# Performance work log

Hardware: AMD Instinct MI355X
Metric: run time of the kernel (lower is better)

## Reference

```python
import jax, jax.numpy as jnp
import numpy as np

LN_EPS = 1e-12
BIG = 1e30
BAND = 15  # end index may be at most 15 tokens after start


def output_layer(x, w1, b1, g, b, w2, b2):
    # Linear -> ReLU -> LayerNorm -> Linear (dropout is identity at eval)
    h = jax.nn.relu(x @ w1 + b1)
    mu = jnp.mean(h, axis=-1, keepdims=True)
    var = jnp.mean(jnp.square(h - mu), axis=-1, keepdims=True)
    h = (h - mu) * jax.lax.rsqrt(var + LN_EPS) * g + b
    return h @ w2 + b2


def setup_inputs() -> dict:
    key = jax.random.key(0)
    ks = jax.random.split(key, 8)
    B, S, D = 8, 4096, 1024
    H2 = 2 * D
    inp = {
        "context_input": jax.random.normal(ks[0], (B, S, D), jnp.float32),
        "context_mask": jnp.ones((B, S), jnp.float32),
    }
    def head(k1, k2, n_ans):
        return (
            0.02 * jax.random.normal(k1, (D, H2), jnp.float32),
            jnp.zeros((H2,), jnp.float32),
            jnp.ones((H2,), jnp.float32),
            jnp.zeros((H2,), jnp.float32),
            0.02 * jax.random.normal(k2, (H2, n_ans), jnp.float32),
            jnp.zeros((n_ans,), jnp.float32),
        )
    for name, k1, k2, n_ans in [("start", ks[1], ks[2], 1), ("end", ks[3], ks[4], 1), ("type", ks[5], ks[6], 4)]:
        w1, b1, g, b, w2, b2 = head(k1, k2, n_ans)
        inp[f"{name}_w1"] = w1; inp[f"{name}_b1"] = b1
        inp[f"{name}_g"] = g; inp[f"{name}_b"] = b
        inp[f"{name}_w2"] = w2; inp[f"{name}_b2"] = b2
    return inp


def reference(context_input, context_mask,
              start_w1, start_b1, start_g, start_b, start_w2, start_b2,
              end_w1, end_b1, end_g, end_b, end_w2, end_b2,
              type_w1, type_b1, type_g, type_b, type_w2, type_b2):
    S = context_input.shape[1]
    start_pred = output_layer(context_input, start_w1, start_b1, start_g, start_b, start_w2, start_b2)[..., 0] \
        - BIG * (1.0 - context_mask)  # [B,S]
    end_pred = output_layer(context_input, end_w1, end_b1, end_g, end_b, end_w2, end_b2)[..., 0] \
        - BIG * (1.0 - context_mask)  # [B,S]
    type_pred = output_layer(context_input[:, 0, :], type_w1, type_b1, type_g, type_b, type_w2, type_b2)  # [B,4]

    # outer[b,i,j] = start[b,i] + end[b,j], masked to band 0 <= j-i <= 15
    outer = start_pred[:, :, None] + end_pred[:, None, :]  # [B,S,S]
    i = jnp.arange(S)[:, None]
    j = jnp.arange(S)[None, :]
    band = ((j >= i) & (j <= i + BAND)).astype(outer.dtype)  # [S,S]
    outer = outer - BIG * (1.0 - band)[None]

    yp1 = jnp.argmax(jnp.max(outer, axis=2), axis=1)  # best start index [B]
    yp2 = jnp.argmax(jnp.max(outer, axis=1), axis=1)  # best end index [B]
    return start_pred, end_pred, type_pred, yp1, yp2
```

## Files before the change

### kernel.cpp

```cpp
#include <hip/hip_runtime.h>

typedef _Float16 f16x8 __attribute__((ext_vector_type(8)));
typedef float f32x4 __attribute__((ext_vector_type(4)));

#define BIGF 1e30f
#define M_TOT 32768
#define H2 2048

#define WS_XH 0u
#define WS_WT 67108864u
#define WS_BVEC 75497472u
#define WS_GW2 75513856u
#define WS_CONSTS 75530240u
#define WS_PART 75530496u
#define WS_TPART 100696320u

__global__ void k_convert_x(const float* __restrict__ x, _Float16* __restrict__ xh) {
  size_t i = ((size_t)blockIdx.x * 256 + threadIdx.x) * 8;
  float4 v0 = *(const float4*)(x + i);
  float4 v1 = *(const float4*)(x + i + 4);
  f16x8 h;
  h[0] = (_Float16)v0.x; h[1] = (_Float16)v0.y; h[2] = (_Float16)v0.z; h[3] = (_Float16)v0.w;
  h[4] = (_Float16)v1.x; h[5] = (_Float16)v1.y; h[6] = (_Float16)v1.z; h[7] = (_Float16)v1.w;
  *(f16x8*)(xh + i) = h;
}

__global__ void k_convert_w(const float* __restrict__ w_s, const float* __restrict__ w_e,
                            _Float16* __restrict__ wt) {
  __shared__ float tile[64][65];
  const float* w = blockIdx.z ? w_e : w_s;
  int n0 = blockIdx.x * 64, k0 = blockIdx.y * 64;
  int tx = threadIdx.x & 63, ty = threadIdx.x >> 6;
#pragma unroll
  for (int i = ty; i < 64; i += 4) tile[i][tx] = w[(size_t)(k0 + i) * H2 + n0 + tx];
  __syncthreads();
#pragma unroll
  for (int i = ty; i < 64; i += 4) {
    wt[((size_t)(blockIdx.z * H2 + n0 + i)) * 1024 + k0 + tx] = (_Float16)tile[tx][i];
  }
}

__global__ void k_prep(const float* __restrict__ s_b1, const float* __restrict__ s_g,
                       const float* __restrict__ s_w2, const float* __restrict__ s_b,
                       const float* __restrict__ s_b2, const float* __restrict__ e_b1,
                       const float* __restrict__ e_g, const float* __restrict__ e_w2,
                       const float* __restrict__ e_b, const float* __restrict__ e_b2,
                       float* __restrict__ bvec, float* __restrict__ gw2,
                       float* __restrict__ consts) {
  int blk = blockIdx.x;
  if (blk < 16) {
    int i = blk * 256 + threadIdx.x;
    int head = i >> 11, j = i & (H2 - 1);
    bvec[i] = head ? e_b1[j] : s_b1[j];
    gw2[i] = head ? e_g[j] * e_w2[j] : s_g[j] * s_w2[j];
  } else {
    int h = blk - 16;
    const float* g = h ? e_g : s_g;
    const float* b = h ? e_b : s_b;
    const float* w2 = h ? e_w2 : s_w2;
    const float* b2 = h ? e_b2 : s_b2;
    float c1 = 0.f, c2 = 0.f;
    for (int j = threadIdx.x; j < H2; j += 256) {
      float w = w2[j];
      c1 += g[j] * w;
      c2 += b[j] * w;
    }
    for (int m = 1; m < 64; m <<= 1) { c1 += __shfl_xor(c1, m); c2 += __shfl_xor(c2, m); }
    __shared__ float r1[4], r2[4];
    int wid = threadIdx.x >> 6;
    if ((threadIdx.x & 63) == 0) { r1[wid] = c1; r2[wid] = c2; }
    __syncthreads();
    if (threadIdx.x == 0) {
      consts[h * 2 + 0] = r1[0] + r1[1] + r1[2] + r1[3];
      consts[h * 2 + 1] = r2[0] + r2[1] + r2[2] + r2[3] + b2[0];
    }
  }
}

#define STA(q, tile)                                                                    \
  __builtin_amdgcn_global_load_lds(                                                     \
      (const __attribute__((address_space(1))) unsigned int*)(srcA + (size_t)(q) * 131072 + (size_t)(tile) * 128), \
      (__attribute__((address_space(3))) unsigned int*)(lds + (q) * 8192 + t * 16), 16, 0, 0)
#define STB(q, tile)                                                                    \
  __builtin_amdgcn_global_load_lds(                                                     \
      (const __attribute__((address_space(1))) unsigned int*)(srcB + (size_t)(q) * 131072 + (size_t)(tile) * 128), \
      (__attribute__((address_space(3))) unsigned int*)(lds + 32768 + (q) * 8192 + t * 16), 16, 0, 0)

#define RD_AB(low)                                                                      \
  _Pragma("unroll")                                                                     \
  for (int i = 0; i < 4; ++i)                                                           \
    af[i] = *(const f16x8*)(lds + arow + i * 2048 + (low));                             \
  _Pragma("unroll")                                                                     \
  for (int nj = 0; nj < 4; ++nj)                                                        \
    bf[nj] = *(const f16x8*)(lds + brow + nj * 2048 + (low));

#define PH_TAIL                                                                         \
  __builtin_amdgcn_sched_barrier(0);                                                    \
  __builtin_amdgcn_s_barrier();                                                         \
  asm volatile("s_waitcnt lgkmcnt(0)" ::: "memory");                                    \
  __builtin_amdgcn_sched_barrier(0);

#define BAR2                                                                            \
  __builtin_amdgcn_sched_barrier(0);                                                    \
  __builtin_amdgcn_s_barrier();                                                         \
  __builtin_amdgcn_sched_barrier(0);

#define MF16                                                                            \
  __builtin_amdgcn_s_setprio(1);                                                        \
  _Pragma("unroll")                                                                     \
  for (int i = 0; i < 4; ++i)                                                           \
    _Pragma("unroll")                                                                   \
    for (int nj = 0; nj < 4; ++nj)                                                      \
      acc[i][nj] = __builtin_amdgcn_mfma_f32_16x16x32_f16(af[i], bf[nj], acc[i][nj], 0, 0, 0); \
  __builtin_amdgcn_s_setprio(0);

__global__ __launch_bounds__(512, 4) void k_gemm(const _Float16* __restrict__ Xh,
                                                 const _Float16* __restrict__ Wt,
                                                 const float* __restrict__ bvec,
                                                 const float* __restrict__ gw2,
                                                 float* __restrict__ partials) {
  __shared__ char lds[49152];
  const int nb = blockIdx.x;
  const int mb = blockIdx.y;
  const int t = threadIdx.x;
  const int lane = t & 63, wid = t >> 6;
  const int c15 = lane & 15, g4 = lane >> 4;
  const int wmg = wid >> 1;
  const int wq = wid & 1;
  const int wn = wq * 64;

  f32x4 acc[4][4];
#pragma unroll
  for (int i = 0; i < 4; ++i)
#pragma unroll
    for (int j = 0; j < 4; ++j) acc[i][j] = (f32x4){0.f, 0.f, 0.f, 0.f};

  const char* Abase = (const char*)(Xh + (size_t)mb * 256 * 1024);
  const char* Bbase = (const char*)(Wt + (size_t)nb * 128 * 1024);
  const int rowl = t >> 3;
  const int swz = ((t & 7) * 16) ^ ((rowl & 7) << 4);
  const char* srcA = Abase + (size_t)rowl * 2048 + swz;
  const char* srcB = Bbase + (size_t)rowl * 2048 + swz;

  const int xorv = (c15 & 7) << 4;
  const int low0 = (g4 * 16) ^ xorv;
  const int low1 = (64 + g4 * 16) ^ xorv;
  const int arow = (wmg * 64 + c15) * 128;
  const int brow = 32768 + (wn + c15) * 128;

  STA(0, 0); STA(1, 0); STA(2, 0); STA(3, 0);
  STB(0, 0); STB(1, 0);
  asm volatile("s_waitcnt vmcnt(0)" ::: "memory");
  __builtin_amdgcn_s_barrier();
  __builtin_amdgcn_sched_barrier(0);

  f16x8 af[4], bf[4];

#pragma unroll
  for (int g = 0; g < 16; ++g) {
    RD_AB(low0)
    PH_TAIL
    MF16
    BAR2
    RD_AB(low1)
    PH_TAIL
    MF16
    BAR2
    if (g < 15) {
      STA(0, g + 1); STA(1, g + 1); STA(2, g + 1); STA(3, g + 1);
      STB(0, g + 1); STB(1, g + 1);
      asm volatile("s_waitcnt vmcnt(0)" ::: "memory");
      __builtin_amdgcn_s_barrier();
      __builtin_amdgcn_sched_barrier(0);
    }
  }

  __syncthreads();
  float* red = (float*)lds;

  float bv[4], gv[4];
#pragma unroll
  for (int nj = 0; nj < 4; ++nj) {
    int col = nb * 128 + wn + nj * 16 + c15;
    bv[nj] = bvec[col];
    gv[nj] = gw2[col];
  }
#pragma unroll
  for (int mi = 0; mi < 4; ++mi) {
#pragma unroll
    for (int r = 0; r < 4; ++r) {
      float s1 = 0.f, s2 = 0.f, s3 = 0.f;
#pragma unroll
      for (int nj = 0; nj < 4; ++nj) {
        float v = acc[mi][nj][r] + bv[nj];
        v = fmaxf(v, 0.f);
        s1 += v;
        s2 += v * v;
        s3 += v * gv[nj];
      }
#pragma unroll
      for (int m = 1; m < 16; m <<= 1) {
        s1 += __shfl_xor(s1, m);
        s2 += __shfl_xor(s2, m);
        s3 += __shfl_xor(s3, m);
      }
      if (c15 == 0) {
        int row = mi * 16 + g4 * 4 + r;
        float* p = red + (((wmg * 2 + wq) * 64 + row) * 3);
        p[0] = s1; p[1] = s2; p[2] = s3;
      }
    }
  }
  __syncthreads();
  for (int idx = t; idx < 768; idx += 512) {
    int wmgi = idx / 192;
    int rem = idx - wmgi * 192;
    int row = rem / 3, k = rem - row * 3;
    float s = red[((wmgi * 2 + 0) * 64 + row) * 3 + k] +
              red[((wmgi * 2 + 1) * 64 + row) * 3 + k];
    int rowg = mb * 256 + wmgi * 64 + row;
    partials[((size_t)(nb * 3 + k)) * M_TOT + rowg] = s;
  }
}

__global__ void k_reduce(const float* __restrict__ partials, const float* __restrict__ consts,
                         const float* __restrict__ mask, float* __restrict__ out) {
  int m = blockIdx.x * 256 + threadIdx.x;
  float s1 = 0.f, s2 = 0.f, s3 = 0.f, e1 = 0.f, e2 = 0.f, e3 = 0.f;
  for (int nb = 0; nb < 16; ++nb) {
    s1 += partials[((size_t)(nb * 3 + 0)) * M_TOT + m];
    s2 += partials[((size_t)(nb * 3 + 1)) * M_TOT + m];
    s3 += partials[((size_t)(nb * 3 + 2)) * M_TOT + m];
  }
  for (int nb = 16; nb < 32; ++nb) {
    e1 += partials[((size_t)(nb * 3 + 0)) * M_TOT + m];
    e2 += partials[((size_t)(nb * 3 + 1)) * M_TOT + m];
    e3 += partials[((size_t)(nb * 3 + 2)) * M_TOT + m];
  }
  const float H = (float)H2;
  float mu = s1 / H;
  float var = fmaxf(s2 / H - mu * mu, 0.f);
  float rs = 1.f / sqrtf(var + 1e-12f);
  float score_s = rs * (s3 - mu * consts[0]) + consts[1];
  mu = e1 / H;
  var = fmaxf(e2 / H - mu * mu, 0.f);
  rs = 1.f / sqrtf(var + 1e-12f);
  float score_e = rs * (e3 - mu * consts[2]) + consts[3];
  float mk = BIGF * (1.f - mask[m]);
  out[m] = score_s - mk;
  out[M_TOT + m] = score_e - mk;
}

__global__ void k_type_partial(const float* __restrict__ X, const float* __restrict__ w1,
                               const float* __restrict__ b1, const float* __restrict__ g,
                               const float* __restrict__ w2, float* __restrict__ tpart) {
  __shared__ float xs[1024];
  int cb = blockIdx.x, tok = blockIdx.y, t = threadIdx.x;
  const float* xp = X + (size_t)tok * 4096 * 1024;
  for (int i = t; i < 1024; i += 256) xs[i] = xp[i];
  __syncthreads();
  int j = cb * 256 + t;
  float dot = 0.f;
  for (int k = 0; k < 1024; ++k) dot += xs[k] * w1[(size_t)k * H2 + j];
  float h = fmaxf(dot + b1[j], 0.f);
  float gj = g[j];
  float s[6];
  s[0] = h;
  s[1] = h * h;
#pragma unroll
  for (int c = 0; c < 4; ++c) s[2 + c] = h * gj * w2[j * 4 + c];
  for (int m = 1; m < 64; m <<= 1)
#pragma unroll
    for (int q = 0; q < 6; ++q) s[q] += __shfl_xor(s[q], m);
  __shared__ float red[4][6];
  int wid = t >> 6;
  if ((t & 63) == 0)
#pragma unroll
    for (int q = 0; q < 6; ++q) red[wid][q] = s[q];
  __syncthreads();
  if (t == 0)
#pragma unroll
    for (int q = 0; q < 6; ++q)
      tpart[(tok * 8 + cb) * 6 + q] = red[0][q] + red[1][q] + red[2][q] + red[3][q];
}

__global__ void k_type_final(const float* __restrict__ tpart, const float* __restrict__ g,
                             const float* __restrict__ bb, const float* __restrict__ w2,
                             const float* __restrict__ b2, float* __restrict__ out) {
  int t = threadIdx.x;
  float c1[4] = {0.f, 0.f, 0.f, 0.f}, c2[4] = {0.f, 0.f, 0.f, 0.f};
  for (int j = t; j < H2; j += 256) {
    float gj = g[j], bj = bb[j];
#pragma unroll
    for (int c = 0; c < 4; ++c) {
      float w = w2[j * 4 + c];
      c1[c] += gj * w;
      c2[c] += bj * w;
    }
  }
  for (int m = 1; m < 64; m <<= 1)
#pragma unroll
    for (int c = 0; c < 4; ++c) { c1[c] += __shfl_xor(c1[c], m); c2[c] += __shfl_xor(c2[c], m); }
  __shared__ float rC1[4][4], rC2[4][4];
  int wid = t >> 6;
  if ((t & 63) == 0)
#pragma unroll
    for (int c = 0; c < 4; ++c) { rC1[wid][c] = c1[c]; rC2[wid][c] = c2[c]; }
  __syncthreads();
  __shared__ float sC1[4], sC2[4];
  if (t < 4) {
    sC1[t] = rC1[0][t] + rC1[1][t] + rC1[2][t] + rC1[3][t];
    sC2[t] = rC2[0][t] + rC2[1][t] + rC2[2][t] + rC2[3][t];
  }
  __syncthreads();
  if (t < 32) {
    int tok = t >> 2, c = t & 3;
    float s1 = 0.f, s2 = 0.f, s3 = 0.f;
    for (int cb = 0; cb < 8; ++cb) {
      s1 += tpart[(tok * 8 + cb) * 6 + 0];
      s2 += tpart[(tok * 8 + cb) * 6 + 1];
      s3 += tpart[(tok * 8 + cb) * 6 + 2 + c];
    }
    float mu = s1 / (float)H2;
    float var = fmaxf(s2 / (float)H2 - mu * mu, 0.f);
    float rs = 1.f / sqrtf(var + 1e-12f);
    out[65536 + tok * 4 + c] = rs * (s3 - mu * sC1[c]) + sC2[c] + b2[c];
  }
}

__global__ void k_band(const float* __restrict__ preds, float* __restrict__ out) {
  __shared__ float ss[4096], se[4096];
  int b = blockIdx.x, t = threadIdx.x;
  for (int i = t; i < 4096; i += 256) {
    ss[i] = preds[(size_t)b * 4096 + i];
    se[i] = preds[M_TOT + (size_t)b * 4096 + i];
  }
  __syncthreads();
  float bv1 = -3.0e38f, bv2 = -3.0e38f;
  int bi1 = 0x7fffffff, bi2 = 0x7fffffff;
  for (int i = t; i < 4096; i += 256) {
    float m1 = -3.0e38f;
    int jmax = i + 15 < 4095 ? i + 15 : 4095;
    for (int j = i; j <= jmax; ++j) m1 = fmaxf(m1, se[j]);
    float v1 = ss[i] + m1;
    if (v1 > bv1 || (v1 == bv1 && i < bi1)) { bv1 = v1; bi1 = i; }
    float m2 = -3.0e38f;
    int imin = i - 15 > 0 ? i - 15 : 0;
    for (int j = imin; j <= i; ++j) m2 = fmaxf(m2, ss[j]);
    float v2 = se[i] + m2;
    if (v2 > bv2 || (v2 == bv2 && i < bi2)) { bv2 = v2; bi2 = i; }
  }
  for (int m = 1; m < 64; m <<= 1) {
    float ov = __shfl_xor(bv1, m);
    int oi = __shfl_xor(bi1, m);
    if (ov > bv1 || (ov == bv1 && oi < bi1)) { bv1 = ov; bi1 = oi; }
    ov = __shfl_xor(bv2, m);
    oi = __shfl_xor(bi2, m);
    if (ov > bv2 || (ov == bv2 && oi < bi2)) { bv2 = ov; bi2 = oi; }
  }
  __shared__ float rv[2][4];
  __shared__ int ri[2][4];
  int wid = t >> 6;
  if ((t & 63) == 0) { rv[0][wid] = bv1; ri[0][wid] = bi1; rv[1][wid] = bv2; ri[1][wid] = bi2; }
  __syncthreads();
  if (t == 0) {
    float v = rv[0][0];
    int ix = ri[0][0];
    for (int w = 1; w < 4; ++w)
      if (rv[0][w] > v || (rv[0][w] == v && ri[0][w] < ix)) { v = rv[0][w]; ix = ri[0][w]; }
    out[65568 + b] = (float)ix;
    v = rv[1][0];
    ix = ri[1][0];
    for (int w = 1; w < 4; ++w)
      if (rv[1][w] > v || (rv[1][w] == v && ri[1][w] < ix)) { v = rv[1][w]; ix = ri[1][w]; }
    out[65576 + b] = (float)ix;
  }
}

extern "C" void kernel_launch(void* const* d_in, const int* in_sizes, int n_in, void* d_out,
                              int out_size, void* d_ws, size_t ws_size, hipStream_t stream) {
  const float* X = (const float*)d_in[0];
  const float* mask = (const float*)d_in[1];
  const float* s_w1 = (const float*)d_in[2];
  const float* s_b1 = (const float*)d_in[3];
  const float* s_g = (const float*)d_in[4];
  const float* s_b = (const float*)d_in[5];
  const float* s_w2 = (const float*)d_in[6];
  const float* s_b2 = (const float*)d_in[7];
  const float* e_w1 = (const float*)d_in[8];
  const float* e_b1 = (const float*)d_in[9];
  const float* e_g = (const float*)d_in[10];
  const float* e_b = (const float*)d_in[11];
  const float* e_w2 = (const float*)d_in[12];
  const float* e_b2 = (const float*)d_in[13];
  const float* t_w1 = (const float*)d_in[14];
  const float* t_b1 = (const float*)d_in[15];
  const float* t_g = (const float*)d_in[16];
  const float* t_b = (const float*)d_in[17];
  const float* t_w2 = (const float*)d_in[18];
  const float* t_b2 = (const float*)d_in[19];

  char* ws = (char*)d_ws;
  _Float16* Xh = (_Float16*)(ws + WS_XH);
  _Float16* Wt = (_Float16*)(ws + WS_WT);
  float* bvec = (float*)(ws + WS_BVEC);
  float* gw2 = (float*)(ws + WS_GW2);
  float* consts = (float*)(ws + WS_CONSTS);
  float* partials = (float*)(ws + WS_PART);
  float* tpart = (float*)(ws + WS_TPART);
  float* out = (float*)d_out;

  k_convert_x<<<16384, 256, 0, stream>>>(X, Xh);
  k_convert_w<<<dim3(32, 16, 2), 256, 0, stream>>>(s_w1, e_w1, Wt);
  k_prep<<<18, 256, 0, stream>>>(s_b1, s_g, s_w2, s_b, s_b2, e_b1, e_g, e_w2, e_b, e_b2,
                                 bvec, gw2, consts);
  k_gemm<<<dim3(32, 128), 512, 0, stream>>>(Xh, Wt, bvec, gw2, partials);
  k_reduce<<<128, 256, 0, stream>>>(partials, consts, mask, out);
  k_type_partial<<<dim3(8, 8), 256, 0, stream>>>(X, t_w1, t_b1, t_g, t_w2, tpart);
  k_type_final<<<1, 256, 0, stream>>>(tpart, t_g, t_b, t_w2, t_b2, out);
  k_band<<<8, 256, 0, stream>>>(out, out);
}
```

Baseline: 454.6 us.

## Use 256x256 GEMM tiles with 32x32 MFMA and double-buffered LDS, merge prep kernels

```diff
diff --git a/kernel.cpp b/kernel.cpp
--- a/kernel.cpp
+++ b/kernel.cpp
@@ -1,7 +1,7 @@
 #include <hip/hip_runtime.h>
 
 typedef _Float16 f16x8 __attribute__((ext_vector_type(8)));
-typedef float f32x4 __attribute__((ext_vector_type(4)));
+typedef float f32x16 __attribute__((ext_vector_type(16)));
 
 #define BIGF 1e30f
 #define M_TOT 32768
@@ -15,164 +15,164 @@
 #define WS_PART 75530496u
 #define WS_TPART 100696320u
 
-__global__ void k_convert_x(const float* __restrict__ x, _Float16* __restrict__ xh) {
-  size_t i = ((size_t)blockIdx.x * 256 + threadIdx.x) * 8;
-  float4 v0 = *(const float4*)(x + i);
-  float4 v1 = *(const float4*)(x + i + 4);
-  f16x8 h;
-  h[0] = (_Float16)v0.x; h[1] = (_Float16)v0.y; h[2] = (_Float16)v0.z; h[3] = (_Float16)v0.w;
-  h[4] = (_Float16)v1.x; h[5] = (_Float16)v1.y; h[6] = (_Float16)v1.z; h[7] = (_Float16)v1.w;
-  *(f16x8*)(xh + i) = h;
-}
-
-__global__ void k_convert_w(const float* __restrict__ w_s, const float* __restrict__ w_e,
-                            _Float16* __restrict__ wt) {
+__global__ void k_pre(const float* __restrict__ x, _Float16* __restrict__ xh,
+                      const float* __restrict__ w_s, const float* __restrict__ w_e,
+                      _Float16* __restrict__ wt,
+                      const float* __restrict__ s_b1, const float* __restrict__ s_g,
+                      const float* __restrict__ s_w2, const float* __restrict__ s_b,
+                      const float* __restrict__ s_b2, const float* __restrict__ e_b1,
+                      const float* __restrict__ e_g, const float* __restrict__ e_w2,
+                      const float* __restrict__ e_b, const float* __restrict__ e_b2,
+                      float* __restrict__ bvec, float* __restrict__ gw2,
+                      float* __restrict__ consts) {
   __shared__ float tile[64][65];
-  const float* w = blockIdx.z ? w_e : w_s;
-  int n0 = blockIdx.x * 64, k0 = blockIdx.y * 64;
-  int tx = threadIdx.x & 63, ty = threadIdx.x >> 6;
-#pragma unroll
-  for (int i = ty; i < 64; i += 4) tile[i][tx] = w[(size_t)(k0 + i) * H2 + n0 + tx];
-  __syncthreads();
-#pragma unroll
-  for (int i = ty; i < 64; i += 4) {
-    wt[((size_t)(blockIdx.z * H2 + n0 + i)) * 1024 + k0 + tx] = (_Float16)tile[tx][i];
-  }
-}
-
-__global__ void k_prep(const float* __restrict__ s_b1, const float* __restrict__ s_g,
-                       const float* __restrict__ s_w2, const float* __restrict__ s_b,
-                       const float* __restrict__ s_b2, const float* __restrict__ e_b1,
-                       const float* __restrict__ e_g, const float* __restrict__ e_w2,
-                       const float* __restrict__ e_b, const float* __restrict__ e_b2,
-                       float* __restrict__ bvec, float* __restrict__ gw2,
-                       float* __restrict__ consts) {
-  int blk = blockIdx.x;
-  if (blk < 16) {
-    int i = blk * 256 + threadIdx.x;
-    int head = i >> 11, j = i & (H2 - 1);
-    bvec[i] = head ? e_b1[j] : s_b1[j];
-    gw2[i] = head ? e_g[j] * e_w2[j] : s_g[j] * s_w2[j];
+  int bid = blockIdx.x;
+  if (bid < 16384) {
+    size_t i = ((size_t)bid * 256 + threadIdx.x) * 8;
+    float4 v0 = *(const float4*)(x + i);
+    float4 v1 = *(const float4*)(x + i + 4);
+    f16x8 h;
+    h[0] = (_Float16)v0.x; h[1] = (_Float16)v0.y; h[2] = (_Float16)v0.z; h[3] = (_Float16)v0.w;
+    h[4] = (_Float16)v1.x; h[5] = (_Float16)v1.y; h[6] = (_Float16)v1.z; h[7] = (_Float16)v1.w;
+    *(f16x8*)(xh + i) = h;
+  } else if (bid < 17408) {
+    int r = bid - 16384;
+    int bx = r & 31, by = (r >> 5) & 15, bz = r >> 9;
+    const float* w = bz ? w_e : w_s;
+    int n0 = bx * 64, k0 = by * 64;
+    int tx = threadIdx.x & 63, ty = threadIdx.x >> 6;
+#pragma unroll
+    for (int i = ty; i < 64; i += 4) tile[i][tx] = w[(size_t)(k0 + i) * H2 + n0 + tx];
+    __syncthreads();
+#pragma unroll
+    for (int i = ty; i < 64; i += 4)
+      wt[((size_t)(bz * H2 + n0 + i)) * 1024 + k0 + tx] = (_Float16)tile[tx][i];
   } else {
-    int h = blk - 16;
-    const float* g = h ? e_g : s_g;
-    const float* b = h ? e_b : s_b;
-    const float* w2 = h ? e_w2 : s_w2;
-    const float* b2 = h ? e_b2 : s_b2;
-    float c1 = 0.f, c2 = 0.f;
-    for (int j = threadIdx.x; j < H2; j += 256) {
-      float w = w2[j];
-      c1 += g[j] * w;
-      c2 += b[j] * w;
+    int blk = bid - 17408;
+    if (blk < 16) {
+      int i = blk * 256 + threadIdx.x;
+      int head = i >> 11, j = i & (H2 - 1);
+      bvec[i] = head ? e_b1[j] : s_b1[j];
+      gw2[i] = head ? e_g[j] * e_w2[j] : s_g[j] * s_w2[j];
+    } else {
+      int h = blk - 16;
+      const float* g = h ? e_g : s_g;
+      const float* b = h ? e_b : s_b;
+      const float* w2 = h ? e_w2 : s_w2;
+      const float* b2 = h ? e_b2 : s_b2;
+      float c1 = 0.f, c2 = 0.f;
+      for (int j = threadIdx.x; j < H2; j += 256) {
+        float w = w2[j];
+        c1 += g[j] * w;
+        c2 += b[j] * w;
+      }
+      for (int m = 1; m < 64; m <<= 1) { c1 += __shfl_xor(c1, m); c2 += __shfl_xor(c2, m); }
+      __shared__ float r1[4], r2[4];
+      int wid = threadIdx.x >> 6;
+      if ((threadIdx.x & 63) == 0) { r1[wid] = c1; r2[wid] = c2; }
+      __syncthreads();
+      if (threadIdx.x == 0) {
+        consts[h * 2 + 0] = r1[0] + r1[1] + r1[2] + r1[3];
+        consts[h * 2 + 1] = r2[0] + r2[1] + r2[2] + r2[3] + b2[0];
+      }
     }
-    for (int m = 1; m < 64; m <<= 1) { c1 += __shfl_xor(c1, m); c2 += __shfl_xor(c2, m); }
-    __shared__ float r1[4], r2[4];
-    int wid = threadIdx.x >> 6;
-    if ((threadIdx.x & 63) == 0) { r1[wid] = c1; r2[wid] = c2; }
-    __syncthreads();
-    if (threadIdx.x == 0) {
-      consts[h * 2 + 0] = r1[0] + r1[1] + r1[2] + r1[3];
-      consts[h * 2 + 1] = r2[0] + r2[1] + r2[2] + r2[3] + b2[0];
-    }
-  }
-}
-
-#define STA(q, tile)                                                                    \
+  }
+}
+
+#define BUF 65536u
+#define STA(q, tile, bufo)                                                              \
   __builtin_amdgcn_global_load_lds(                                                     \
-      (const __attribute__((address_space(1))) unsigned int*)(srcA + (size_t)(q) * 131072 + (size_t)(tile) * 128), \
-      (__attribute__((address_space(3))) unsigned int*)(lds + (q) * 8192 + t * 16), 16, 0, 0)
-#define STB(q, tile)                                                                    \
+      (const __attribute__((address_space(1))) unsigned int*)(srcA + (size_t)(q) * 65536 + (size_t)(tile) * 128), \
+      (__attribute__((address_space(3))) unsigned int*)(lds + (bufo) + (q) * 4096 + t * 16), 16, 0, 0)
+#define STB(q, tile, bufo)                                                              \
   __builtin_amdgcn_global_load_lds(                                                     \
-      (const __attribute__((address_space(1))) unsigned int*)(srcB + (size_t)(q) * 131072 + (size_t)(tile) * 128), \
-      (__attribute__((address_space(3))) unsigned int*)(lds + 32768 + (q) * 8192 + t * 16), 16, 0, 0)
-
-#define RD_AB(low)                                                                      \
+      (const __attribute__((address_space(1))) unsigned int*)(srcB + (size_t)(q) * 65536 + (size_t)(tile) * 128), \
+      (__attribute__((address_space(3))) unsigned int*)(lds + (bufo) + 32768u + (q) * 4096 + t * 16), 16, 0, 0)
+#define STAGE_TILE(tile, bufo)                                                          \
+  _Pragma("unroll")                                                                     \
+  for (int q = 0; q < 8; ++q) { STA(q, tile, bufo); STB(q, tile, bufo); }
+
+#define RDF(AF, BF, s, bufo)                                                            \
   _Pragma("unroll")                                                                     \
   for (int i = 0; i < 4; ++i)                                                           \
-    af[i] = *(const f16x8*)(lds + arow + i * 2048 + (low));                             \
+    AF[i] = *(const f16x8*)(lds + (bufo) + (unsigned)((wm + i * 32 + l31) * 128) +      \
+                            (unsigned)((((s) * 32) + hi16) ^ xorv));                    \
   _Pragma("unroll")                                                                     \
-  for (int nj = 0; nj < 4; ++nj)                                                        \
-    bf[nj] = *(const f16x8*)(lds + brow + nj * 2048 + (low));
-
-#define PH_TAIL                                                                         \
-  __builtin_amdgcn_sched_barrier(0);                                                    \
-  __builtin_amdgcn_s_barrier();                                                         \
-  asm volatile("s_waitcnt lgkmcnt(0)" ::: "memory");                                    \
-  __builtin_amdgcn_sched_barrier(0);
-
-#define BAR2                                                                            \
-  __builtin_amdgcn_sched_barrier(0);                                                    \
-  __builtin_amdgcn_s_barrier();                                                         \
-  __builtin_amdgcn_sched_barrier(0);
-
-#define MF16                                                                            \
+  for (int j = 0; j < 4; ++j)                                                           \
+    BF[j] = *(const f16x8*)(lds + (bufo) + 32768u + (unsigned)((wn + j * 32 + l31) * 128) + \
+                            (unsigned)((((s) * 32) + hi16) ^ xorv));
+
+#define MF(AF, BF)                                                                      \
   __builtin_amdgcn_s_setprio(1);                                                        \
   _Pragma("unroll")                                                                     \
   for (int i = 0; i < 4; ++i)                                                           \
     _Pragma("unroll")                                                                   \
-    for (int nj = 0; nj < 4; ++nj)                                                      \
-      acc[i][nj] = __builtin_amdgcn_mfma_f32_16x16x32_f16(af[i], bf[nj], acc[i][nj], 0, 0, 0); \
+    for (int j = 0; j < 4; ++j)                                                         \
+      acc[i][j] = __builtin_amdgcn_mfma_f32_32x32x16_f16(AF[i], BF[j], acc[i][j], 0, 0, 0); \
   __builtin_amdgcn_s_setprio(0);
 
-__global__ __launch_bounds__(512, 4) void k_gemm(const _Float16* __restrict__ Xh,
+__global__ __launch_bounds__(256, 1) void k_gemm(const _Float16* __restrict__ Xh,
                                                  const _Float16* __restrict__ Wt,
                                                  const float* __restrict__ bvec,
                                                  const float* __restrict__ gw2,
                                                  float* __restrict__ partials) {
-  __shared__ char lds[49152];
+  __shared__ char lds[2 * BUF];
   const int nb = blockIdx.x;
   const int mb = blockIdx.y;
   const int t = threadIdx.x;
   const int lane = t & 63, wid = t >> 6;
-  const int c15 = lane & 15, g4 = lane >> 4;
-  const int wmg = wid >> 1;
-  const int wq = wid & 1;
-  const int wn = wq * 64;
-
-  f32x4 acc[4][4];
+  const int l31 = lane & 31, hi = lane >> 5;
+  const int hi16 = hi * 16;
+  const int wm = (wid >> 1) * 128;
+  const int wn = (wid & 1) * 128;
+
+  f32x16 acc[4][4];
 #pragma unroll
   for (int i = 0; i < 4; ++i)
 #pragma unroll
-    for (int j = 0; j < 4; ++j) acc[i][j] = (f32x4){0.f, 0.f, 0.f, 0.f};
+    for (int j = 0; j < 4; ++j)
+#pragma unroll
+      for (int r = 0; r < 16; ++r) acc[i][j][r] = 0.f;
 
   const char* Abase = (const char*)(Xh + (size_t)mb * 256 * 1024);
-  const char* Bbase = (const char*)(Wt + (size_t)nb * 128 * 1024);
+  const char* Bbase = (const char*)(Wt + (size_t)nb * 256 * 1024);
   const int rowl = t >> 3;
   const int swz = ((t & 7) * 16) ^ ((rowl & 7) << 4);
   const char* srcA = Abase + (size_t)rowl * 2048 + swz;
   const char* srcB = Bbase + (size_t)rowl * 2048 + swz;
 
-  const int xorv = (c15 & 7) << 4;
-  const int low0 = (g4 * 16) ^ xorv;
-  const int low1 = (64 + g4 * 16) ^ xorv;
-  const int arow = (wmg * 64 + c15) * 128;
-  const int brow = 32768 + (wn + c15) * 128;
-
-  STA(0, 0); STA(1, 0); STA(2, 0); STA(3, 0);
-  STB(0, 0); STB(1, 0);
-  asm volatile("s_waitcnt vmcnt(0)" ::: "memory");
+  const int xorv = (l31 & 7) << 4;
+
+  STAGE_TILE(0, 0u)
+  STAGE_TILE(1, BUF)
+  asm volatile("s_waitcnt vmcnt(16)" ::: "memory");
   __builtin_amdgcn_s_barrier();
   __builtin_amdgcn_sched_barrier(0);
 
-  f16x8 af[4], bf[4];
-
-#pragma unroll
+  f16x8 A0[4], B0[4], A1[4], B1[4];
+  RDF(A0, B0, 0, 0u)
+
+#pragma unroll 2
   for (int g = 0; g < 16; ++g) {
-    RD_AB(low0)
-    PH_TAIL
-    MF16
-    BAR2
-    RD_AB(low1)
-    PH_TAIL
-    MF16
-    BAR2
-    if (g < 15) {
-      STA(0, g + 1); STA(1, g + 1); STA(2, g + 1); STA(3, g + 1);
-      STB(0, g + 1); STB(1, g + 1);
-      asm volatile("s_waitcnt vmcnt(0)" ::: "memory");
-      __builtin_amdgcn_s_barrier();
-      __builtin_amdgcn_sched_barrier(0);
-    }
+    const unsigned ob = (unsigned)(g & 1) * BUF;
+    const unsigned on = ob ^ BUF;
+    RDF(A1, B1, 1, ob)
+    MF(A0, B0)
+    RDF(A0, B0, 2, ob)
+    MF(A1, B1)
+    RDF(A1, B1, 3, ob)
+    MF(A0, B0)
+    MF(A1, B1)
+    __builtin_amdgcn_sched_barrier(0);
+    __builtin_amdgcn_s_barrier();
+    __builtin_amdgcn_sched_barrier(0);
+    if (g < 14) { STAGE_TILE(g + 2, ob) }
+    if (g < 14)       asm volatile("s_waitcnt vmcnt(16)" ::: "memory");
+    else if (g == 14) asm volatile("s_waitcnt vmcnt(0)" ::: "memory");
+    __builtin_amdgcn_sched_barrier(0);
+    __builtin_amdgcn_s_barrier();
+    __builtin_amdgcn_sched_barrier(0);
+    if (g < 15) { RDF(A0, B0, 0, on) }
   }
 
   __syncthreads();
@@ -181,44 +181,44 @@
   float bv[4], gv[4];
 #pragma unroll
   for (int nj = 0; nj < 4; ++nj) {
-    int col = nb * 128 + wn + nj * 16 + c15;
+    int col = nb * 256 + wn + nj * 32 + l31;
     bv[nj] = bvec[col];
     gv[nj] = gw2[col];
   }
 #pragma unroll
   for (int mi = 0; mi < 4; ++mi) {
 #pragma unroll
-    for (int r = 0; r < 4; ++r) {
+    for (int reg = 0; reg < 16; ++reg) {
       float s1 = 0.f, s2 = 0.f, s3 = 0.f;
 #pragma unroll
       for (int nj = 0; nj < 4; ++nj) {
-        float v = acc[mi][nj][r] + bv[nj];
+        float v = acc[mi][nj][reg] + bv[nj];
         v = fmaxf(v, 0.f);
         s1 += v;
         s2 += v * v;
         s3 += v * gv[nj];
       }
 #pragma unroll
-      for (int m = 1; m < 16; m <<= 1) {
+      for (int m = 1; m < 32; m <<= 1) {
         s1 += __shfl_xor(s1, m);
         s2 += __shfl_xor(s2, m);
         s3 += __shfl_xor(s3, m);
       }
-      if (c15 == 0) {
-        int row = mi * 16 + g4 * 4 + r;
-        float* p = red + (((wmg * 2 + wq) * 64 + row) * 3);
+      if (l31 == 0) {
+        int row_local = mi * 32 + (reg & 3) + 8 * (reg >> 2) + 4 * hi;
+        float* p = red + ((wid * 128 + row_local) * 3);
         p[0] = s1; p[1] = s2; p[2] = s3;
       }
     }
   }
   __syncthreads();
-  for (int idx = t; idx < 768; idx += 512) {
-    int wmgi = idx / 192;
-    int rem = idx - wmgi * 192;
+  for (int idx = t; idx < 768; idx += 256) {
+    int half = idx / 384;
+    int rem = idx - half * 384;
     int row = rem / 3, k = rem - row * 3;
-    float s = red[((wmgi * 2 + 0) * 64 + row) * 3 + k] +
-              red[((wmgi * 2 + 1) * 64 + row) * 3 + k];
-    int rowg = mb * 256 + wmgi * 64 + row;
+    float s = red[((half * 2 + 0) * 128 + row) * 3 + k] +
+              red[((half * 2 + 1) * 128 + row) * 3 + k];
+    int rowg = mb * 256 + half * 128 + row;
     partials[((size_t)(nb * 3 + k)) * M_TOT + rowg] = s;
   }
 }
@@ -227,12 +227,12 @@
                          const float* __restrict__ mask, float* __restrict__ out) {
   int m = blockIdx.x * 256 + threadIdx.x;
   float s1 = 0.f, s2 = 0.f, s3 = 0.f, e1 = 0.f, e2 = 0.f, e3 = 0.f;
-  for (int nb = 0; nb < 16; ++nb) {
+  for (int nb = 0; nb < 8; ++nb) {
     s1 += partials[((size_t)(nb * 3 + 0)) * M_TOT + m];
     s2 += partials[((size_t)(nb * 3 + 1)) * M_TOT + m];
     s3 += partials[((size_t)(nb * 3 + 2)) * M_TOT + m];
   }
-  for (int nb = 16; nb < 32; ++nb) {
+  for (int nb = 8; nb < 16; ++nb) {
     e1 += partials[((size_t)(nb * 3 + 0)) * M_TOT + m];
     e2 += partials[((size_t)(nb * 3 + 1)) * M_TOT + m];
     e3 += partials[((size_t)(nb * 3 + 2)) * M_TOT + m];
@@ -410,11 +410,9 @@
   float* tpart = (float*)(ws + WS_TPART);
   float* out = (float*)d_out;
 
-  k_convert_x<<<16384, 256, 0, stream>>>(X, Xh);
-  k_convert_w<<<dim3(32, 16, 2), 256, 0, stream>>>(s_w1, e_w1, Wt);
-  k_prep<<<18, 256, 0, stream>>>(s_b1, s_g, s_w2, s_b, s_b2, e_b1, e_g, e_w2, e_b, e_b2,
-                                 bvec, gw2, consts);
-  k_gemm<<<dim3(32, 128), 512, 0, stream>>>(Xh, Wt, bvec, gw2, partials);
+  k_pre<<<17426, 256, 0, stream>>>(X, Xh, s_w1, e_w1, Wt, s_b1, s_g, s_w2, s_b, s_b2,
+                                   e_b1, e_g, e_w2, e_b, e_b2, bvec, gw2, consts);
+  k_gemm<<<dim3(16, 128), 256, 0, stream>>>(Xh, Wt, bvec, gw2, partials);
   k_reduce<<<128, 256, 0, stream>>>(partials, consts, mask, out);
   k_type_partial<<<dim3(8, 8), 256, 0, stream>>>(X, t_w1, t_b1, t_g, t_w2, tpart);
   k_type_final<<<1, 256, 0, stream>>>(tpart, t_g, t_b, t_w2, t_b2, out);
```

Result: slower. 1.382 ms (+204.1%).
